# Performance work log

Measured on AMD Instinct MI355X. Metric: run time of the kernel, lower is better.

The kernel has to match this reference:

```python
import jax, jax.numpy as jnp
import numpy as np

TOP_K = 8
NUM_EXPERTS = 256
HIDDEN = 7168
NUM_TOKENS = 16384
NORM_TOPK_PROB = True


def setup_inputs() -> dict:
    key = jax.random.key(0)
    k1, k2 = jax.random.split(key)
    hidden_states = jax.random.normal(k1, (NUM_TOKENS, HIDDEN), dtype=jnp.float32)
    weight = jax.random.normal(k2, (NUM_EXPERTS, HIDDEN), dtype=jnp.float32) * 0.02
    return {"hidden_states": hidden_states, "weight": weight}


def reference(hidden_states, weight):
    # Router logits: [T, E] = [T, H] @ [E, H]^T
    logits = jnp.einsum("th,eh->te", hidden_states, weight)
    # Fused softmax + top-k (npu_moe_gating_top_k_softmax semantics):
    # softmax over experts, then take top-k probabilities and their indices.
    probs = jax.nn.softmax(logits, axis=-1)
    topk_weight, topk_idx = jax.lax.top_k(probs, TOP_K)  # [T, k]
    # row_idx: expert-major (column-major) flattened row indices, as the NPU op returns.
    T = logits.shape[0]
    row_idx = jnp.arange(T * TOP_K, dtype=jnp.int32).reshape(TOP_K, T).T  # [T, k]
    if TOP_K > 1 and NORM_TOPK_PROB:
        denominator = jnp.sum(topk_weight, axis=-1, keepdims=True) + 1e-20
        topk_weight = topk_weight / denominator
    topk_idx = topk_idx.astype(jnp.int32)
    return (topk_idx, topk_weight, row_idx)
```

## Files before the change

### kernel.cpp

```cpp
#include <hip/hip_runtime.h>
#include <hip/hip_bf16.h>

#define NTOK 16384
#define HID 7168
#define NEXP 256
#define TOPK 8

#define BT 64
#define BK 128
#define NPH (HID / BK)

typedef __bf16 bf16x8 __attribute__((ext_vector_type(8)));
typedef float  f32x16 __attribute__((ext_vector_type(16)));

typedef __attribute__((address_space(1))) const unsigned char ga_t;
typedef __attribute__((address_space(3))) unsigned char la_t;

__device__ __align__(16) unsigned short g_wb[NEXP * HID];

__device__ __forceinline__ unsigned int f2bfb(float x) {
    unsigned int u = __float_as_uint(x);
    return (u + 0x7fffu + ((u >> 16) & 1u)) >> 16;
}
__device__ __forceinline__ uint4 pk4(float4 p, float4 q) {
    uint4 u;
    u.x = f2bfb(p.x) | (f2bfb(p.y) << 16);
    u.y = f2bfb(p.z) | (f2bfb(p.w) << 16);
    u.z = f2bfb(q.x) | (f2bfb(q.y) << 16);
    u.w = f2bfb(q.z) | (f2bfb(q.w) << 16);
    return u;
}
__device__ __forceinline__ bf16x8 asbf8(uint4 u) {
    union { uint4 a; bf16x8 b; } c; c.a = u; return c.b;
}
__device__ __forceinline__ void gll16(const void* g, void* l) {
    __builtin_amdgcn_global_load_lds((ga_t*)g, (la_t*)l, 16, 0, 0);
}
__device__ __forceinline__ bf16x8 cvt8(float4 p, float4 q) {
    union { bf16x8 v; __hip_bfloat162 h[4]; } c;
    c.h[0] = __float22bfloat162_rn(make_float2(p.x, p.y));
    c.h[1] = __float22bfloat162_rn(make_float2(p.z, p.w));
    c.h[2] = __float22bfloat162_rn(make_float2(q.x, q.y));
    c.h[3] = __float22bfloat162_rn(make_float2(q.z, q.w));
    return c.v;
}

__global__ void wconv_frag(const float* __restrict__ wt) {
    const int tid = blockIdx.x * 256 + threadIdx.x;
    const int l  = tid & 63;
    const int ks = (tid >> 6) & 7;
    const int g  = (tid >> 9) & 7;
    const int p  = tid >> 12;
    const int e  = g * 32 + (l & 31);
    const int kb = p * 128 + ks * 16 + ((l >> 5) << 3);
    const float4* s = (const float4*)(wt + (size_t)e * HID + kb);
    ((uint4*)g_wb)[tid] = pk4(s[0], s[1]);
}

__global__ void moe_rows(float* __restrict__ ob) {
    const int q = blockIdx.x * 256 + threadIdx.x;
    ob[262144 + q] = (float)((q & 7) * NTOK + (q >> 3));
}

__global__ __launch_bounds__(512) void moe_gate_v12(
    const float* __restrict__ hs,
    float* __restrict__ ob)
{
    __shared__ __align__(16) char smem[66560];
    char* const bufA0 = smem;
    char* const bufA1 = smem + 32768;

    const int tid  = threadIdx.x;
    const int t0   = blockIdx.x * BT;
    const int lane = tid & 63;
    const int wv   = tid >> 6;
    const int wm   = wv >> 2;
    const int wn   = wv & 3;

    const char* aS[4];
    int aD[4];
    #pragma unroll
    for (int i = 0; i < 4; ++i) {
        const int r2 = (wv * 4 + i) * 2 + (lane >> 5);
        const int cs = ((lane & 31) * 16) ^ ((r2 & 31) << 4);
        aS[i] = (const char*)hs + (size_t)(t0 + r2) * HID * 4 + cs;
        aD[i] = (wv * 4 + i) * 1024;
    }

    const int khalf = lane >> 5;
    const int rowA  = wm * 32 + (lane & 31);
    const int abase = rowA * 512;
    const int aswz  = (rowA & 31) << 4;

    const char* const wbB = (const char*)g_wb + (size_t)(wn * 2) * 8192 + lane * 16;

    f32x16 acc0 = {};
    f32x16 acc1 = {};

    uint4 s0[16];
    uint4 s1[16];

#define ISSUE_A(P, BUF)                                                       \
    do {                                                                      \
        _Pragma("unroll")                                                     \
        for (int i = 0; i < 4; ++i)                                           \
            gll16(aS[i] + (size_t)(P) * 512, (BUF) + aD[i]);                  \
        __builtin_amdgcn_sched_barrier(0);                                    \
    } while (0)

#define ISSUE_B(P, ARR)                                                       \
    do {                                                                      \
        const char* bp = wbB + (size_t)(P) * 65536;                           \
        _Pragma("unroll")                                                     \
        for (int c = 0; c < 2; ++c)                                           \
            _Pragma("unroll")                                                 \
            for (int ks = 0; ks < 8; ++ks)                                    \
                ARR[c * 8 + ks] = *(const uint4*)(bp + c * 8192 + ks * 1024); \
        __builtin_amdgcn_sched_barrier(0);                                    \
    } while (0)

#define COMPUTE(BUF, ARR)                                                     \
    do {                                                                      \
        _Pragma("unroll")                                                     \
        for (int ks = 0; ks < 8; ++ks) {                                      \
            const int o = ks * 64 + khalf * 32;                               \
            float4 a0 = *(const float4*)((BUF) + abase + ((o     ) ^ aswz));  \
            float4 a1 = *(const float4*)((BUF) + abase + ((o + 16) ^ aswz));  \
            bf16x8 a = cvt8(a0, a1);                                          \
            acc0 = __builtin_amdgcn_mfma_f32_32x32x16_bf16(a, asbf8(ARR[ks]),     acc0, 0, 0, 0); \
            acc1 = __builtin_amdgcn_mfma_f32_32x32x16_bf16(a, asbf8(ARR[8 + ks]), acc1, 0, 0, 0); \
        }                                                                     \
    } while (0)

#define WAITBAR(VM)                                                           \
    do {                                                                      \
        asm volatile("s_waitcnt vmcnt(" #VM ")" ::: "memory");                \
        __builtin_amdgcn_sched_barrier(0);                                    \
        __builtin_amdgcn_s_barrier();                                         \
        __builtin_amdgcn_sched_barrier(0);                                    \
    } while (0)

#define ENDBAR()                                                              \
    do {                                                                      \
        __builtin_amdgcn_s_barrier();                                         \
        __builtin_amdgcn_sched_barrier(0);                                    \
    } while (0)

    ISSUE_B(0, s0);
    ISSUE_A(0, bufA0);
    ISSUE_A(1, bufA1);

    for (int p = 0; p < 54; p += 2) {
        ISSUE_B(p + 1, s1);
        WAITBAR(20);
        COMPUTE(bufA0, s0);
        ENDBAR();
        ISSUE_A(p + 2, bufA0);

        ISSUE_B(p + 2, s0);
        WAITBAR(20);
        COMPUTE(bufA1, s1);
        ENDBAR();
        if (p + 3 < NPH) ISSUE_A(p + 3, bufA1);
    }
    ISSUE_B(55, s1);
    WAITBAR(20);
    COMPUTE(bufA0, s0);
    ENDBAR();
    WAITBAR(0);
    COMPUTE(bufA1, s1);
    __syncthreads();

    float* ll = (float*)smem;
    {
        const int ec = wn * 64 + (lane & 31);
        const int rb = wm * 32 + 4 * (lane >> 5);
        #pragma unroll
        for (int r = 0; r < 16; ++r) {
            const int tok = rb + (r & 3) + 8 * (r >> 2);
            ll[tok * 257 + ec]      = acc0[r];
            ll[tok * 257 + ec + 32] = acc1[r];
        }
    }
    __syncthreads();

    if (tid < BT) {
        const float* lr = ll + tid * 257;
        float bv[TOPK]; int bi8[TOPK];
        #pragma unroll
        for (int k = 0; k < TOPK; ++k) { bv[k] = -1e30f; bi8[k] = 0; }
        for (int e = 0; e < NEXP; ++e) {
            const float v = lr[e];
            if (v > bv[TOPK - 1]) {
                int k = TOPK - 1;
                while (k > 0 && v > bv[k - 1]) {
                    bv[k] = bv[k - 1]; bi8[k] = bi8[k - 1]; --k;
                }
                bv[k] = v; bi8[k] = e;
            }
        }
        float ev[TOPK], ssum = 0.f;
        #pragma unroll
        for (int r = 0; r < TOPK; ++r) { ev[r] = expf(bv[r] - bv[0]); ssum += ev[r]; }
        const float inv = 1.0f / ssum;

        const int tg = t0 + tid;
        #pragma unroll
        for (int r = 0; r < TOPK; ++r) {
            ob[(size_t)tg * TOPK + r]          = (float)bi8[r];
            ob[131072 + (size_t)tg * TOPK + r] = ev[r] * inv;
        }
    }
#undef ISSUE_A
#undef ISSUE_B
#undef COMPUTE
#undef WAITBAR
#undef ENDBAR
}

extern "C" void kernel_launch(void* const* d_in, const int* in_sizes, int n_in,
                              void* d_out, int out_size, void* d_ws, size_t ws_size,
                              hipStream_t stream) {
    const float* hs = (const float*)d_in[0];
    const float* wt = (const float*)d_in[1];
    float* ob = (float*)d_out;

    wconv_frag<<<dim3(NEXP * HID / 8 / 256), dim3(256), 0, stream>>>(wt);
    moe_gate_v12<<<dim3(NTOK / BT), dim3(512), 0, stream>>>(hs, ob);
    moe_rows<<<dim3(512), dim3(256), 0, stream>>>(ob);
}
```

Baseline: 248.3 us.

## Give each wave private A buffers with 4-deep pipeline and drop block barriers

Reworks the gating GEMM so each of 4 waves owns a private 32KB LDS ring of four 8KB A stages and computes 32 tokens x 128 experts, with BK halved to 64. Because waves stage their own activations, the per-phase block-wide s_barriers go away and only vmcnt waits remain. Each wave also gets deeper prefetch of A. The cost is 128KB LDS per block with 256 threads, which lowers occupancy and doubles the B fragment loads per wave relative to its compute share.

```diff
diff --git a/kernel.cpp b/kernel.cpp
--- a/kernel.cpp
+++ b/kernel.cpp
@@ -6,8 +6,7 @@
 #define NEXP 256
 #define TOPK 8
 
-#define BT 64
-#define BK 128
+#define BK 64
 #define NPH (HID / BK)
 
 typedef __bf16 bf16x8 __attribute__((ext_vector_type(8)));
@@ -62,129 +61,129 @@
     ob[262144 + q] = (float)((q & 7) * NTOK + (q >> 3));
 }
 
-__global__ __launch_bounds__(512) void moe_gate_v12(
+__global__ __launch_bounds__(256) void moe_gate_v13(
     const float* __restrict__ hs,
     float* __restrict__ ob)
 {
-    __shared__ __align__(16) char smem[66560];
-    char* const bufA0 = smem;
-    char* const bufA1 = smem + 32768;
-
-    const int tid  = threadIdx.x;
-    const int t0   = blockIdx.x * BT;
-    const int lane = tid & 63;
-    const int wv   = tid >> 6;
-    const int wm   = wv >> 2;
-    const int wn   = wv & 3;
-
-    const char* aS[4];
-    int aD[4];
+    __shared__ __align__(16) char smem[131072];
+
+    const int tid   = threadIdx.x;
+    const int lane  = tid & 63;
+    const int w     = tid >> 6;
+    const int tg    = w >> 1;
+    const int h     = w & 1;
+    const int tw0   = blockIdx.x * 64 + tg * 32;
+    char* const wbuf = smem + w * 32768;
+
+    const char* aSrc[4];
     #pragma unroll
     for (int i = 0; i < 4; ++i) {
-        const int r2 = (wv * 4 + i) * 2 + (lane >> 5);
-        const int cs = ((lane & 31) * 16) ^ ((r2 & 31) << 4);
-        aS[i] = (const char*)hs + (size_t)(t0 + r2) * HID * 4 + cs;
-        aD[i] = (wv * 4 + i) * 1024;
-    }
+        const int row = 4 * i + (lane >> 4);
+        const int cs  = (((lane & 15) << 4) ^ ((row & 15) << 4));
+        aSrc[i] = (const char*)hs + (size_t)(tw0 + row) * (HID * 4) + cs;
+    }
+    const size_t AHI = (size_t)16 * HID * 4;
+
+    const char* const bB = (const char*)g_wb + h * 32768 + lane * 16;
 
     const int khalf = lane >> 5;
-    const int rowA  = wm * 32 + (lane & 31);
-    const int abase = rowA * 512;
-    const int aswz  = (rowA & 31) << 4;
-
-    const char* const wbB = (const char*)g_wb + (size_t)(wn * 2) * 8192 + lane * 16;
-
-    f32x16 acc0 = {};
-    f32x16 acc1 = {};
-
-    uint4 s0[16];
-    uint4 s1[16];
-
-#define ISSUE_A(P, BUF)                                                       \
-    do {                                                                      \
+    const int abase = (lane & 31) * 256;
+    const int aswz  = ((lane & 31) & 15) << 4;
+
+    f32x16 acc0 = {}, acc1 = {}, acc2 = {}, acc3 = {};
+    uint4 b0[16], b1[16];
+
+#define ISSUE_A(Q, SLOT)                                                      \
+    do {                                                                      \
+        char* dst = wbuf + ((SLOT) << 13);                                    \
         _Pragma("unroll")                                                     \
         for (int i = 0; i < 4; ++i)                                           \
-            gll16(aS[i] + (size_t)(P) * 512, (BUF) + aD[i]);                  \
+            gll16(aSrc[i] + (size_t)(Q) * 256, dst + i * 1024);               \
+        _Pragma("unroll")                                                     \
+        for (int i = 0; i < 4; ++i)                                           \
+            gll16(aSrc[i] + AHI + (size_t)(Q) * 256, dst + 4096 + i * 1024);  \
+    } while (0)
+
+#define ISSUE_B(BP, SET)                                                      \
+    do {                                                                      \
+        _Pragma("unroll")                                                     \
+        for (int j = 0; j < 4; ++j)                                           \
+            _Pragma("unroll")                                                 \
+            for (int ks = 0; ks < 4; ++ks)                                    \
+                SET[j * 4 + ks] = *(const uint4*)((BP) + j * 8192 + ks * 1024); \
+    } while (0)
+
+#define COMPUTE(BUFP, SET)                                                    \
+    do {                                                                      \
+        _Pragma("unroll")                                                     \
+        for (int ks = 0; ks < 4; ++ks) {                                      \
+            const int o = ks * 64 + khalf * 32;                               \
+            float4 a0 = *(const float4*)((BUFP) + abase + ((o     ) ^ aswz)); \
+            float4 a1 = *(const float4*)((BUFP) + abase + ((o + 16) ^ aswz)); \
+            bf16x8 a = cvt8(a0, a1);                                          \
+            acc0 = __builtin_amdgcn_mfma_f32_32x32x16_bf16(a, asbf8(SET[     ks]), acc0, 0, 0, 0); \
+            acc1 = __builtin_amdgcn_mfma_f32_32x32x16_bf16(a, asbf8(SET[ 4 + ks]), acc1, 0, 0, 0); \
+            acc2 = __builtin_amdgcn_mfma_f32_32x32x16_bf16(a, asbf8(SET[ 8 + ks]), acc2, 0, 0, 0); \
+            acc3 = __builtin_amdgcn_mfma_f32_32x32x16_bf16(a, asbf8(SET[12 + ks]), acc3, 0, 0, 0); \
+        }                                                                     \
+    } while (0)
+
+#define VMW(N)                                                                \
+    do {                                                                      \
+        asm volatile("s_waitcnt vmcnt(" #N ")" ::: "memory");                 \
         __builtin_amdgcn_sched_barrier(0);                                    \
     } while (0)
 
-#define ISSUE_B(P, ARR)                                                       \
-    do {                                                                      \
-        const char* bp = wbB + (size_t)(P) * 65536;                           \
-        _Pragma("unroll")                                                     \
-        for (int c = 0; c < 2; ++c)                                           \
-            _Pragma("unroll")                                                 \
-            for (int ks = 0; ks < 8; ++ks)                                    \
-                ARR[c * 8 + ks] = *(const uint4*)(bp + c * 8192 + ks * 1024); \
-        __builtin_amdgcn_sched_barrier(0);                                    \
-    } while (0)
-
-#define COMPUTE(BUF, ARR)                                                     \
-    do {                                                                      \
-        _Pragma("unroll")                                                     \
-        for (int ks = 0; ks < 8; ++ks) {                                      \
-            const int o = ks * 64 + khalf * 32;                               \
-            float4 a0 = *(const float4*)((BUF) + abase + ((o     ) ^ aswz));  \
-            float4 a1 = *(const float4*)((BUF) + abase + ((o + 16) ^ aswz));  \
-            bf16x8 a = cvt8(a0, a1);                                          \
-            acc0 = __builtin_amdgcn_mfma_f32_32x32x16_bf16(a, asbf8(ARR[ks]),     acc0, 0, 0, 0); \
-            acc1 = __builtin_amdgcn_mfma_f32_32x32x16_bf16(a, asbf8(ARR[8 + ks]), acc1, 0, 0, 0); \
-        }                                                                     \
-    } while (0)
-
-#define WAITBAR(VM)                                                           \
-    do {                                                                      \
-        asm volatile("s_waitcnt vmcnt(" #VM ")" ::: "memory");                \
-        __builtin_amdgcn_sched_barrier(0);                                    \
-        __builtin_amdgcn_s_barrier();                                         \
-        __builtin_amdgcn_sched_barrier(0);                                    \
-    } while (0)
-
-#define ENDBAR()                                                              \
-    do {                                                                      \
-        __builtin_amdgcn_s_barrier();                                         \
-        __builtin_amdgcn_sched_barrier(0);                                    \
-    } while (0)
-
-    ISSUE_B(0, s0);
-    ISSUE_A(0, bufA0);
-    ISSUE_A(1, bufA1);
-
-    for (int p = 0; p < 54; p += 2) {
-        ISSUE_B(p + 1, s1);
-        WAITBAR(20);
-        COMPUTE(bufA0, s0);
-        ENDBAR();
-        ISSUE_A(p + 2, bufA0);
-
-        ISSUE_B(p + 2, s0);
-        WAITBAR(20);
-        COMPUTE(bufA1, s1);
-        ENDBAR();
-        if (p + 3 < NPH) ISSUE_A(p + 3, bufA1);
-    }
-    ISSUE_B(55, s1);
-    WAITBAR(20);
-    COMPUTE(bufA0, s0);
-    ENDBAR();
-    WAITBAR(0);
-    COMPUTE(bufA1, s1);
+    ISSUE_A(0, 0);
+    ISSUE_B(bB, b0);
+    ISSUE_A(1, 1);
+
+    const char* bpi = bB;
+    for (int p = 0; p < 108; p += 2) {
+        ISSUE_B(bpi + 4096, b1);
+        ISSUE_A(p + 2, ((p + 2) & 3));
+        VMW(32);
+        COMPUTE(wbuf + ((p & 3) << 13), b0);
+        ISSUE_B(bpi + 65536, b0);
+        ISSUE_A(p + 3, ((p + 3) & 3));
+        VMW(32);
+        COMPUTE(wbuf + (((p + 1) & 3) << 13), b1);
+        bpi += 65536;
+    }
+    ISSUE_B(bpi + 4096, b1);
+    ISSUE_A(110, 2);
+    VMW(32);
+    COMPUTE(wbuf + (0 << 13), b0);
+    ISSUE_B(bpi + 65536, b0);
+    ISSUE_A(111, 3);
+    VMW(32);
+    COMPUTE(wbuf + (1 << 13), b1);
+    ISSUE_B(bpi + 65536 + 4096, b1);
+    VMW(24);
+    COMPUTE(wbuf + (2 << 13), b0);
+    VMW(0);
+    COMPUTE(wbuf + (3 << 13), b1);
+
     __syncthreads();
 
     float* ll = (float*)smem;
     {
-        const int ec = wn * 64 + (lane & 31);
-        const int rb = wm * 32 + 4 * (lane >> 5);
-        #pragma unroll
-        for (int r = 0; r < 16; ++r) {
-            const int tok = rb + (r & 3) + 8 * (r >> 2);
-            ll[tok * 257 + ec]      = acc0[r];
-            ll[tok * 257 + ec + 32] = acc1[r];
+        const int rb = 4 * khalf;
+        #pragma unroll
+        for (int j = 0; j < 4; ++j) {
+            const int ec = h * 128 + j * 32 + (lane & 31);
+            #pragma unroll
+            for (int r = 0; r < 16; ++r) {
+                const int tok = tg * 32 + (r & 3) + 8 * (r >> 2) + rb;
+                const float v = (j == 0) ? acc0[r] : (j == 1) ? acc1[r]
+                              : (j == 2) ? acc2[r] : acc3[r];
+                ll[tok * 257 + ec] = v;
+            }
         }
     }
     __syncthreads();
 
-    if (tid < BT) {
+    if (tid < 64) {
         const float* lr = ll + tid * 257;
         float bv[TOPK]; int bi8[TOPK];
         #pragma unroll
@@ -204,18 +203,17 @@
         for (int r = 0; r < TOPK; ++r) { ev[r] = expf(bv[r] - bv[0]); ssum += ev[r]; }
         const float inv = 1.0f / ssum;
 
-        const int tg = t0 + tid;
+        const int tgl = blockIdx.x * 64 + tid;
         #pragma unroll
         for (int r = 0; r < TOPK; ++r) {
-            ob[(size_t)tg * TOPK + r]          = (float)bi8[r];
-            ob[131072 + (size_t)tg * TOPK + r] = ev[r] * inv;
+            ob[(size_t)tgl * TOPK + r]          = (float)bi8[r];
+            ob[131072 + (size_t)tgl * TOPK + r] = ev[r] * inv;
         }
     }
 #undef ISSUE_A
 #undef ISSUE_B
 #undef COMPUTE
-#undef WAITBAR
-#undef ENDBAR
+#undef VMW
 }
 
 extern "C" void kernel_launch(void* const* d_in, const int* in_sizes, int n_in,
@@ -226,6 +224,6 @@
     float* ob = (float*)d_out;
 
     wconv_frag<<<dim3(NEXP * HID / 8 / 256), dim3(256), 0, stream>>>(wt);
-    moe_gate_v12<<<dim3(NTOK / BT), dim3(512), 0, stream>>>(hs, ob);
+    moe_gate_v13<<<dim3(NTOK / 64), dim3(256), 0, stream>>>(hs, ob);
     moe_rows<<<dim3(512), dim3(256), 0, stream>>>(ob);
 }
```

New measurement: 261.1 us. 1.05x slower.

## Shrink token tile to 32 with bf16 LDS staging and triple-buffered pipeline

Applied to the files above, without the earlier changes.

The gating GEMM kernel drops from 64-token to 32-token blocks, with each of 8 waves owning 32 experts and a single accumulator. Activations are now loaded through registers, converted to bf16 once and written to a triple-buffered LDS ring in 64-wide K steps. This replaces the direct global-to-LDS fp32 loads and the per-wave conversion. The smaller LDS footprint and the launch bounds hint aim at higher occupancy and twice the number of blocks. In exchange, the weight operand is reread by twice as many blocks, and there is a barrier every 64 K elements.

```diff
diff --git a/kernel.cpp b/kernel.cpp
--- a/kernel.cpp
+++ b/kernel.cpp
@@ -6,15 +6,11 @@
 #define NEXP 256
 #define TOPK 8
 
-#define BT 64
-#define BK 128
-#define NPH (HID / BK)
+#define BT 32
+#define NIT 112
 
 typedef __bf16 bf16x8 __attribute__((ext_vector_type(8)));
 typedef float  f32x16 __attribute__((ext_vector_type(16)));
-
-typedef __attribute__((address_space(1))) const unsigned char ga_t;
-typedef __attribute__((address_space(3))) unsigned char la_t;
 
 __device__ __align__(16) unsigned short g_wb[NEXP * HID];
 
@@ -32,17 +28,6 @@
 }
 __device__ __forceinline__ bf16x8 asbf8(uint4 u) {
     union { uint4 a; bf16x8 b; } c; c.a = u; return c.b;
-}
-__device__ __forceinline__ void gll16(const void* g, void* l) {
-    __builtin_amdgcn_global_load_lds((ga_t*)g, (la_t*)l, 16, 0, 0);
-}
-__device__ __forceinline__ bf16x8 cvt8(float4 p, float4 q) {
-    union { bf16x8 v; __hip_bfloat162 h[4]; } c;
-    c.h[0] = __float22bfloat162_rn(make_float2(p.x, p.y));
-    c.h[1] = __float22bfloat162_rn(make_float2(p.z, p.w));
-    c.h[2] = __float22bfloat162_rn(make_float2(q.x, q.y));
-    c.h[3] = __float22bfloat162_rn(make_float2(q.z, q.w));
-    return c.v;
 }
 
 __global__ void wconv_frag(const float* __restrict__ wt) {
@@ -62,124 +47,101 @@
     ob[262144 + q] = (float)((q & 7) * NTOK + (q >> 3));
 }
 
-__global__ __launch_bounds__(512) void moe_gate_v12(
+__global__ __launch_bounds__(512, 4) void moe_gate_v15(
     const float* __restrict__ hs,
     float* __restrict__ ob)
 {
-    __shared__ __align__(16) char smem[66560];
-    char* const bufA0 = smem;
-    char* const bufA1 = smem + 32768;
+    __shared__ __align__(16) char smem[33792];
 
-    const int tid  = threadIdx.x;
-    const int t0   = blockIdx.x * BT;
-    const int lane = tid & 63;
-    const int wv   = tid >> 6;
-    const int wm   = wv >> 2;
-    const int wn   = wv & 3;
+    const int tid   = threadIdx.x;
+    const int lane  = tid & 63;
+    const int w     = tid >> 6;
+    const int khalf = lane >> 5;
+    const int t0    = blockIdx.x * BT;
 
-    const char* aS[4];
-    int aD[4];
-    #pragma unroll
-    for (int i = 0; i < 4; ++i) {
-        const int r2 = (wv * 4 + i) * 2 + (lane >> 5);
-        const int cs = ((lane & 31) * 16) ^ ((r2 & 31) << 4);
-        aS[i] = (const char*)hs + (size_t)(t0 + r2) * HID * 4 + cs;
-        aD[i] = (wv * 4 + i) * 1024;
-    }
+    const int ar = tid >> 4;
+    const int ac = tid & 15;
+    const float* aload = hs + (size_t)(t0 + ar) * HID + ac * 4;
+    const int awb = (ac >> 1) * 512 + ar * 16 + (ac & 1) * 8;
 
-    const int khalf = lane >> 5;
-    const int rowA  = wm * 32 + (lane & 31);
-    const int abase = rowA * 512;
-    const int aswz  = (rowA & 31) << 4;
+    const int arb = (lane & 31) * 16;
 
-    const char* const wbB = (const char*)g_wb + (size_t)(wn * 2) * 8192 + lane * 16;
+    const char* const bbase = (const char*)g_wb + w * 8192 + lane * 16;
 
-    f32x16 acc0 = {};
-    f32x16 acc1 = {};
+    f32x16 acc = {};
+    uint4 bA0, bA1, bA2, bA3;
+    uint4 bB0, bB1, bB2, bB3;
 
-    uint4 s0[16];
-    uint4 s1[16];
+    char* p0 = smem;
+    char* p1 = smem + 4096;
+    char* p2 = smem + 8192;
 
-#define ISSUE_A(P, BUF)                                                       \
+#define LOADB(SET, S)                                                         \
     do {                                                                      \
-        _Pragma("unroll")                                                     \
-        for (int i = 0; i < 4; ++i)                                           \
-            gll16(aS[i] + (size_t)(P) * 512, (BUF) + aD[i]);                  \
-        __builtin_amdgcn_sched_barrier(0);                                    \
+        const char* bp = bbase + (size_t)((S) >> 1) * 65536 + ((S) & 1) * 4096; \
+        b##SET##0 = *(const uint4*)(bp);                                      \
+        b##SET##1 = *(const uint4*)(bp + 1024);                               \
+        b##SET##2 = *(const uint4*)(bp + 2048);                               \
+        b##SET##3 = *(const uint4*)(bp + 3072);                               \
     } while (0)
 
-#define ISSUE_B(P, ARR)                                                       \
+#define WRITEA(V, BUF)                                                        \
     do {                                                                      \
-        const char* bp = wbB + (size_t)(P) * 65536;                           \
-        _Pragma("unroll")                                                     \
-        for (int c = 0; c < 2; ++c)                                           \
-            _Pragma("unroll")                                                 \
-            for (int ks = 0; ks < 8; ++ks)                                    \
-                ARR[c * 8 + ks] = *(const uint4*)(bp + c * 8192 + ks * 1024); \
-        __builtin_amdgcn_sched_barrier(0);                                    \
+        uint2 u;                                                              \
+        u.x = f2bfb((V).x) | (f2bfb((V).y) << 16);                            \
+        u.y = f2bfb((V).z) | (f2bfb((V).w) << 16);                            \
+        *(uint2*)((BUF) + awb) = u;                                           \
     } while (0)
 
-#define COMPUTE(BUF, ARR)                                                     \
+#define COMPUTE(BUF, SET)                                                     \
     do {                                                                      \
-        _Pragma("unroll")                                                     \
-        for (int ks = 0; ks < 8; ++ks) {                                      \
-            const int o = ks * 64 + khalf * 32;                               \
-            float4 a0 = *(const float4*)((BUF) + abase + ((o     ) ^ aswz));  \
-            float4 a1 = *(const float4*)((BUF) + abase + ((o + 16) ^ aswz));  \
-            bf16x8 a = cvt8(a0, a1);                                          \
-            acc0 = __builtin_amdgcn_mfma_f32_32x32x16_bf16(a, asbf8(ARR[ks]),     acc0, 0, 0, 0); \
-            acc1 = __builtin_amdgcn_mfma_f32_32x32x16_bf16(a, asbf8(ARR[8 + ks]), acc1, 0, 0, 0); \
-        }                                                                     \
+        bf16x8 a;                                                             \
+        a = *(const bf16x8*)((BUF) + (0 * 2 + khalf) * 512 + arb);            \
+        acc = __builtin_amdgcn_mfma_f32_32x32x16_bf16(a, asbf8(b##SET##0), acc, 0, 0, 0); \
+        a = *(const bf16x8*)((BUF) + (1 * 2 + khalf) * 512 + arb);            \
+        acc = __builtin_amdgcn_mfma_f32_32x32x16_bf16(a, asbf8(b##SET##1), acc, 0, 0, 0); \
+        a = *(const bf16x8*)((BUF) + (2 * 2 + khalf) * 512 + arb);            \
+        acc = __builtin_amdgcn_mfma_f32_32x32x16_bf16(a, asbf8(b##SET##2), acc, 0, 0, 0); \
+        a = *(const bf16x8*)((BUF) + (3 * 2 + khalf) * 512 + arb);            \
+        acc = __builtin_amdgcn_mfma_f32_32x32x16_bf16(a, asbf8(b##SET##3), acc, 0, 0, 0); \
     } while (0)
 
-#define WAITBAR(VM)                                                           \
-    do {                                                                      \
-        asm volatile("s_waitcnt vmcnt(" #VM ")" ::: "memory");                \
-        __builtin_amdgcn_sched_barrier(0);                                    \
-        __builtin_amdgcn_s_barrier();                                         \
-        __builtin_amdgcn_sched_barrier(0);                                    \
-    } while (0)
+    {
+        float4 v0 = *(const float4*)(aload);
+        float4 v1 = *(const float4*)(aload + 64);
+        WRITEA(v0, p0);
+        WRITEA(v1, p1);
+    }
+    LOADB(A, 0);
+    __syncthreads();
 
-#define ENDBAR()                                                              \
-    do {                                                                      \
-        __builtin_amdgcn_s_barrier();                                         \
-        __builtin_amdgcn_sched_barrier(0);                                    \
-    } while (0)
+    for (int s = 0; s < NIT; s += 2) {
+        float4 vA;
+        const bool ldA = (s + 2 < NIT);
+        if (ldA) vA = *(const float4*)(aload + (size_t)(s + 2) * 64);
+        LOADB(B, s + 1);
+        COMPUTE(p0, A);
+        __syncthreads();
+        if (ldA) WRITEA(vA, p2);
 
-    ISSUE_B(0, s0);
-    ISSUE_A(0, bufA0);
-    ISSUE_A(1, bufA1);
+        float4 vB;
+        const bool ldB = (s + 3 < NIT);
+        if (ldB) vB = *(const float4*)(aload + (size_t)(s + 3) * 64);
+        if (s + 2 < NIT) LOADB(A, s + 2);
+        COMPUTE(p1, B);
+        __syncthreads();
+        if (ldB) WRITEA(vB, p0);
 
-    for (int p = 0; p < 54; p += 2) {
-        ISSUE_B(p + 1, s1);
-        WAITBAR(20);
-        COMPUTE(bufA0, s0);
-        ENDBAR();
-        ISSUE_A(p + 2, bufA0);
-
-        ISSUE_B(p + 2, s0);
-        WAITBAR(20);
-        COMPUTE(bufA1, s1);
-        ENDBAR();
-        if (p + 3 < NPH) ISSUE_A(p + 3, bufA1);
+        char* t = p2; p2 = p1; p1 = p0; p0 = t;
     }
-    ISSUE_B(55, s1);
-    WAITBAR(20);
-    COMPUTE(bufA0, s0);
-    ENDBAR();
-    WAITBAR(0);
-    COMPUTE(bufA1, s1);
-    __syncthreads();
 
     float* ll = (float*)smem;
     {
-        const int ec = wn * 64 + (lane & 31);
-        const int rb = wm * 32 + 4 * (lane >> 5);
+        const int ec = w * 32 + (lane & 31);
         #pragma unroll
         for (int r = 0; r < 16; ++r) {
-            const int tok = rb + (r & 3) + 8 * (r >> 2);
-            ll[tok * 257 + ec]      = acc0[r];
-            ll[tok * 257 + ec + 32] = acc1[r];
+            const int tok = (r & 3) + 8 * (r >> 2) + 4 * khalf;
+            ll[tok * 257 + ec] = acc[r];
         }
     }
     __syncthreads();
@@ -211,11 +173,9 @@
             ob[131072 + (size_t)tg * TOPK + r] = ev[r] * inv;
         }
     }
-#undef ISSUE_A
-#undef ISSUE_B
+#undef LOADB
+#undef WRITEA
 #undef COMPUTE
-#undef WAITBAR
-#undef ENDBAR
 }
 
 extern "C" void kernel_launch(void* const* d_in, const int* in_sizes, int n_in,
@@ -226,6 +186,6 @@
     float* ob = (float*)d_out;
 
     wconv_frag<<<dim3(NEXP * HID / 8 / 256), dim3(256), 0, stream>>>(wt);
-    moe_gate_v12<<<dim3(NTOK / BT), dim3(512), 0, stream>>>(hs, ob);
+    moe_gate_v15<<<dim3(NTOK / BT), dim3(512), 0, stream>>>(hs, ob);
     moe_rows<<<dim3(512), dim3(256), 0, stream>>>(ob);
 }
```

After: 242.5 us, median of 3. 1.02x faster.
